# Kernel optimization log

Hardware: AMD Instinct MI355X
Metric: run time of the kernel (lower is better)

Reference implementation:

```python
import jax, jax.numpy as jnp
import numpy as np


def setup_inputs() -> dict:
    key = jax.random.key(0)
    k1, k2 = jax.random.split(key)
    B, N, M, D = 4, 8192, 8192, 3
    prediction = jax.random.normal(k1, (B, N, D), dtype=jnp.float32)
    target = jax.random.normal(k2, (B, M, D), dtype=jnp.float32)
    return {"prediction": prediction, "target": target}


def reference(prediction, target):
    # prediction: [B, N, 3], target: [B, M, 3] (already channels-last,
    # matching the module's transpose-if-needed behavior).
    x2 = jnp.sum(prediction * prediction, axis=-1)  # [B, N]
    y2 = jnp.sum(target * target, axis=-1)          # [B, M]
    xy = jnp.einsum('bnd,bmd->bnm', prediction, target)  # [B, N, M]
    d2 = x2[:, :, None] + y2[:, None, :] - 2.0 * xy
    d2 = jnp.maximum(d2, 0.0)  # numerical guard
    # pytorch3d chamfer_distance defaults: point_reduction='mean',
    # batch_reduction='mean' -> mean over points per direction, mean over batch,
    # then sum the two directions.
    cham_x = jnp.min(d2, axis=2).mean()  # pred -> target
    cham_y = jnp.min(d2, axis=1).mean()  # target -> pred
    return cham_x + cham_y
```

## Files before the change

### kernel.cpp

```cpp
#include <hip/hip_runtime.h>


#define BLOCK 256
#define RPT   8
#define MC    256
#define NPTS  8192
#define NCH   (NPTS / MC)
#define NB    4

typedef float v2f __attribute__((ext_vector_type(2)));
typedef float v4f __attribute__((ext_vector_type(4)));

__device__ __forceinline__ float min3f(float a, float b, float c) {
    float d;
    asm("v_min3_f32 %0, %1, %2, %3" : "=v"(d) : "v"(a), "v"(b), "v"(c));
    return d;
}

__device__ __forceinline__ v2f pk_fma(v2f a, v2f b, v2f c) {
    v2f d;
    asm("v_pk_fma_f32 %0, %1, %2, %3" : "=v"(d) : "v"(a), "v"(b), "v"(c));
    return d;
}

__global__ __launch_bounds__(BLOCK) void chamfer_min_fused(
    const float* __restrict__ pred, const float* __restrict__ targ,
    float* __restrict__ pA,
    float* __restrict__ pB,
    double* __restrict__ acc, unsigned int* __restrict__ counter) {
    if (blockIdx.x == 0 && blockIdx.y == 0 && blockIdx.z == 0 && threadIdx.x == 0) {
        *acc = 0.0;
        *counter = 0u;
    }

    const int z   = blockIdx.z;
    const int dir = z >> 2, b = z & (NB - 1);
    const float* X = dir ? targ : pred;
    const float* Y = dir ? pred : targ;
    float* partial = dir ? pB : pA;

    __shared__ v4f ldsA[MC / 2];
    __shared__ v4f ldsB[MC / 2];
    const int mc = blockIdx.y;

    if (threadIdx.x < MC / 2) {
        const int p = threadIdx.x;
        const float* yp = Y + ((size_t)b * NPTS + (size_t)mc * MC + 2 * p) * 3;
        float ax = yp[0], ay = yp[1], az = yp[2];
        float bx = yp[3], by = yp[4], bz = yp[5];
        float aw = fmaf(ax, ax, fmaf(ay, ay, az * az));
        float bw = fmaf(bx, bx, fmaf(by, by, bz * bz));
        ldsA[p] = (v4f){ax, bx, ay, by};
        ldsB[p] = (v4f){az, bz, aw, bw};
    }
    __syncthreads();

    const int row0 = blockIdx.x * (BLOCK * RPT);
    v2f qx[RPT], qy[RPT], qz[RPT];
    float x2[RPT], best[RPT];
#pragma unroll
    for (int r = 0; r < RPT; ++r) {
        int row = row0 + r * BLOCK + threadIdx.x;
        const float* xp = X + ((size_t)b * NPTS + row) * 3;
        float px = xp[0], py = xp[1], pz = xp[2];
        qx[r] = (v2f){-2.0f * px, -2.0f * px};
        qy[r] = (v2f){-2.0f * py, -2.0f * py};
        qz[r] = (v2f){-2.0f * pz, -2.0f * pz};
        x2[r] = fmaf(px, px, fmaf(py, py, pz * pz));
        best[r] = 3.0e38f;
    }

#pragma unroll 2
    for (int j = 0; j < MC / 2; j += 2) {
        v4f A0 = ldsA[j],     B0 = ldsB[j];
        v4f A1 = ldsA[j + 1], B1 = ldsB[j + 1];
        v2f x01 = __builtin_shufflevector(A0, A0, 0, 1);
        v2f y01 = __builtin_shufflevector(A0, A0, 2, 3);
        v2f z01 = __builtin_shufflevector(B0, B0, 0, 1);
        v2f w01 = __builtin_shufflevector(B0, B0, 2, 3);
        v2f x23 = __builtin_shufflevector(A1, A1, 0, 1);
        v2f y23 = __builtin_shufflevector(A1, A1, 2, 3);
        v2f z23 = __builtin_shufflevector(B1, B1, 0, 1);
        v2f w23 = __builtin_shufflevector(B1, B1, 2, 3);
#pragma unroll
        for (int r = 0; r < RPT; ++r) {
            v2f c01 = pk_fma(qx[r], x01, pk_fma(qy[r], y01, pk_fma(qz[r], z01, w01)));
            v2f c23 = pk_fma(qx[r], x23, pk_fma(qy[r], y23, pk_fma(qz[r], z23, w23)));
            best[r] = min3f(best[r], c01.x, c01.y);
            best[r] = min3f(best[r], c23.x, c23.y);
        }
    }

#pragma unroll
    for (int r = 0; r < RPT; ++r) {
        int row = row0 + r * BLOCK + threadIdx.x;
        partial[((size_t)b * NCH + mc) * NPTS + row] = fmaxf(best[r] + x2[r], 0.0f);
    }
}

__global__ __launch_bounds__(256) void chamfer_reduce(
    const float* __restrict__ pA, const float* __restrict__ pB,
    double* __restrict__ acc, unsigned int* __restrict__ counter,
    float* __restrict__ out) {
    const int g = blockIdx.x * 256 + threadIdx.x;
    const int r4 = g * 4;
    const int half = NB * NPTS;
    const float* src = (r4 < half) ? pA : pB;
    const int gg = r4 & (half - 1);
    const int b = gg >> 13, r = gg & (NPTS - 1);

    v4f vb = (v4f){3.0e38f, 3.0e38f, 3.0e38f, 3.0e38f};
#pragma unroll 8
    for (int c = 0; c < NCH; ++c) {
        v4f v = *(const v4f*)(src + ((size_t)b * NCH + c) * NPTS + r);
        vb.x = fminf(vb.x, v.x);
        vb.y = fminf(vb.y, v.y);
        vb.z = fminf(vb.z, v.z);
        vb.w = fminf(vb.w, v.w);
    }

    double d = (double)vb.x + (double)vb.y + (double)vb.z + (double)vb.w;
    for (int off = 32; off > 0; off >>= 1) d += __shfl_down(d, off);
    __shared__ double sh[4];
    const int lane = threadIdx.x & 63, wid = threadIdx.x >> 6;
    if (lane == 0) sh[wid] = d;
    __syncthreads();

    if (threadIdx.x == 0) {
        double blocktotal = sh[0] + sh[1] + sh[2] + sh[3];
        atomicAdd(acc, blocktotal);
        __threadfence();
        unsigned int ticket = atomicAdd(counter, 1u);
        if (ticket == gridDim.x - 1) {
            __threadfence();
            double s = atomicAdd(acc, 0.0);
            out[0] = (float)(s / (double)(NB * NPTS));
        }
    }
}

extern "C" void kernel_launch(void* const* d_in, const int* in_sizes, int n_in,
                              void* d_out, int out_size, void* d_ws, size_t ws_size,
                              hipStream_t stream) {
    const float* pred = (const float*)d_in[0];
    const float* targ = (const float*)d_in[1];
    float* out = (float*)d_out;

    float* pA = (float*)d_ws;
    float* pB = pA + (size_t)NB * NCH * NPTS;
    double* acc = (double*)(pB + (size_t)NB * NCH * NPTS);
    unsigned int* counter = (unsigned int*)(acc + 1);

    dim3 g1(NPTS / (BLOCK * RPT), NCH, 2 * NB);
    chamfer_min_fused<<<g1, BLOCK, 0, stream>>>(pred, targ, pA, pB, acc, counter);

    const int nblk = (2 * NB * NPTS / 4) / 256;
    chamfer_reduce<<<nblk, 256, 0, stream>>>(pA, pB, acc, counter, out);
}
```

Before: 99.83 us.

## Pre-pack target points and stream them via scalar loads instead of LDS

Adds a pack kernel that precomputes squared norms and interleaves each group of four points into 64-byte records in workspace. The main kernel then drops its LDS staging and barrier, and streams these records into SGPRs with double-buffered s_load_dwordx16 so the packed FMAs take scalar operands. The aim is to remove LDS read traffic and the block sync from the inner loop. The cost is an extra kernel launch and explicit waitcnt serialisation on scalar loads every group.

```diff
diff --git a/kernel.cpp b/kernel.cpp
--- a/kernel.cpp
+++ b/kernel.cpp
@@ -7,53 +7,66 @@
 #define NPTS  8192
 #define NCH   (NPTS / MC)
 #define NB    4
+#define NGRP  (NPTS / 4)
+#define GPC   (MC / 4)
 
-typedef float v2f __attribute__((ext_vector_type(2)));
-typedef float v4f __attribute__((ext_vector_type(4)));
+typedef float v2f  __attribute__((ext_vector_type(2)));
+typedef float v4f  __attribute__((ext_vector_type(4)));
+typedef int   v16i __attribute__((ext_vector_type(16)));
 
 __device__ __forceinline__ float min3f(float a, float b, float c) {
     float d;
     asm("v_min3_f32 %0, %1, %2, %3" : "=v"(d) : "v"(a), "v"(b), "v"(c));
     return d;
 }
-
-__device__ __forceinline__ v2f pk_fma(v2f a, v2f b, v2f c) {
+__device__ __forceinline__ v2f pk_fma_vvs(v2f a, v2f b, v2f c) {
     v2f d;
-    asm("v_pk_fma_f32 %0, %1, %2, %3" : "=v"(d) : "v"(a), "v"(b), "v"(c));
+    asm("v_pk_fma_f32 %0, %1, %2, %3" : "=v"(d) : "v"(a), "v"(b), "s"(c));
+    return d;
+}
+__device__ __forceinline__ v2f pk_fma_vsv(v2f a, v2f b, v2f c) {
+    v2f d;
+    asm("v_pk_fma_f32 %0, %1, %2, %3" : "=v"(d) : "v"(a), "s"(b), "v"(c));
     return d;
 }
 
-__global__ __launch_bounds__(BLOCK) void chamfer_min_fused(
+__global__ __launch_bounds__(256) void pack_kernel(
     const float* __restrict__ pred, const float* __restrict__ targ,
+    float* __restrict__ pk, double* __restrict__ acc,
+    unsigned int* __restrict__ counter) {
+    const int t = blockIdx.x * 256 + threadIdx.x;
+    if (t == 0) { *acc = 0.0; *counter = 0u; }
+    const int dir = t / (NB * NGRP);
+    const int rem = t % (NB * NGRP);
+    const int b = rem / NGRP, g = rem % NGRP;
+    const float* Y = dir ? pred : targ;
+    const float* yp = Y + ((size_t)b * NPTS + (size_t)g * 4) * 3;
+    float out[16];
+#pragma unroll
+    for (int i = 0; i < 4; ++i) {
+        float x = yp[3 * i], y = yp[3 * i + 1], z = yp[3 * i + 2];
+        float w = fmaf(x, x, fmaf(y, y, z * z));
+        int base = (i >> 1) * 8, sub = i & 1;
+        out[base + 0 + sub] = x;
+        out[base + 2 + sub] = y;
+        out[base + 4 + sub] = w;
+        out[base + 6 + sub] = z;
+    }
+    v4f* dst = (v4f*)(pk + (size_t)t * 16);
+    const v4f* o = (const v4f*)out;
+    dst[0] = o[0]; dst[1] = o[1]; dst[2] = o[2]; dst[3] = o[3];
+}
+
+__global__ __launch_bounds__(BLOCK) void chamfer_min_smem(
+    const float* __restrict__ pred, const float* __restrict__ targ,
+    const float* __restrict__ pk,
     float* __restrict__ pA,
-    float* __restrict__ pB,
-    double* __restrict__ acc, unsigned int* __restrict__ counter) {
-    if (blockIdx.x == 0 && blockIdx.y == 0 && blockIdx.z == 0 && threadIdx.x == 0) {
-        *acc = 0.0;
-        *counter = 0u;
-    }
-
-    const int z   = blockIdx.z;
+    float* __restrict__ pB) {
+    const int z = blockIdx.z;
     const int dir = z >> 2, b = z & (NB - 1);
     const float* X = dir ? targ : pred;
-    const float* Y = dir ? pred : targ;
     float* partial = dir ? pB : pA;
-
-    __shared__ v4f ldsA[MC / 2];
-    __shared__ v4f ldsB[MC / 2];
     const int mc = blockIdx.y;
-
-    if (threadIdx.x < MC / 2) {
-        const int p = threadIdx.x;
-        const float* yp = Y + ((size_t)b * NPTS + (size_t)mc * MC + 2 * p) * 3;
-        float ax = yp[0], ay = yp[1], az = yp[2];
-        float bx = yp[3], by = yp[4], bz = yp[5];
-        float aw = fmaf(ax, ax, fmaf(ay, ay, az * az));
-        float bw = fmaf(bx, bx, fmaf(by, by, bz * bz));
-        ldsA[p] = (v4f){ax, bx, ay, by};
-        ldsB[p] = (v4f){az, bz, aw, bw};
-    }
-    __syncthreads();
 
     const int row0 = blockIdx.x * (BLOCK * RPT);
     v2f qx[RPT], qy[RPT], qz[RPT];
@@ -70,26 +83,39 @@
         best[r] = 3.0e38f;
     }
 
-#pragma unroll 2
-    for (int j = 0; j < MC / 2; j += 2) {
-        v4f A0 = ldsA[j],     B0 = ldsB[j];
-        v4f A1 = ldsA[j + 1], B1 = ldsB[j + 1];
-        v2f x01 = __builtin_shufflevector(A0, A0, 0, 1);
-        v2f y01 = __builtin_shufflevector(A0, A0, 2, 3);
-        v2f z01 = __builtin_shufflevector(B0, B0, 0, 1);
-        v2f w01 = __builtin_shufflevector(B0, B0, 2, 3);
-        v2f x23 = __builtin_shufflevector(A1, A1, 0, 1);
-        v2f y23 = __builtin_shufflevector(A1, A1, 2, 3);
-        v2f z23 = __builtin_shufflevector(B1, B1, 0, 1);
-        v2f w23 = __builtin_shufflevector(B1, B1, 2, 3);
-#pragma unroll
-        for (int r = 0; r < RPT; ++r) {
-            v2f c01 = pk_fma(qx[r], x01, pk_fma(qy[r], y01, pk_fma(qz[r], z01, w01)));
-            v2f c23 = pk_fma(qx[r], x23, pk_fma(qy[r], y23, pk_fma(qz[r], z23, w23)));
-            best[r] = min3f(best[r], c01.x, c01.y);
-            best[r] = min3f(best[r], c23.x, c23.y);
-        }
+#define AS2(S, i, j) (v2f){__int_as_float(S[i]), __int_as_float(S[j])}
+#define COMPUTE(S) do {                                                   \
+        v2f x01 = AS2(S, 0, 1),  y01 = AS2(S, 2, 3);                      \
+        v2f w01 = AS2(S, 4, 5),  z01 = AS2(S, 6, 7);                      \
+        v2f x23 = AS2(S, 8, 9),  y23 = AS2(S, 10, 11);                    \
+        v2f w23 = AS2(S, 12, 13), z23 = AS2(S, 14, 15);                   \
+        _Pragma("unroll")                                                 \
+        for (int r = 0; r < RPT; ++r) {                                   \
+            v2f t0 = pk_fma_vvs(qz[r], z01, w01);                         \
+            t0 = pk_fma_vsv(qy[r], y01, t0);                              \
+            t0 = pk_fma_vsv(qx[r], x01, t0);                              \
+            v2f t1 = pk_fma_vvs(qz[r], z23, w23);                         \
+            t1 = pk_fma_vsv(qy[r], y23, t1);                              \
+            t1 = pk_fma_vsv(qx[r], x23, t1);                              \
+            best[r] = min3f(best[r], t0.x, t0.y);                         \
+            best[r] = min3f(best[r], t1.x, t1.y);                         \
+        }                                                                 \
+    } while (0)
+
+    const float* base = pk + (((size_t)dir * NB + b) * NGRP + (size_t)mc * GPC) * 16;
+    v16i cur, nxt;
+    asm volatile("s_load_dwordx16 %0, %1, 0x0" : "=s"(cur) : "s"(base));
+    asm volatile("s_waitcnt lgkmcnt(0)" ::: "memory");
+    __builtin_amdgcn_sched_barrier(0);
+    for (int j = 0; j < GPC - 1; ++j) {
+        asm volatile("s_load_dwordx16 %0, %1, 0x40" : "=s"(nxt) : "s"(base));
+        COMPUTE(cur);
+        asm volatile("s_waitcnt lgkmcnt(0)" ::: "memory");
+        __builtin_amdgcn_sched_barrier(0);
+        cur = nxt;
+        base += 16;
     }
+    COMPUTE(cur);
 
 #pragma unroll
     for (int r = 0; r < RPT; ++r) {
@@ -148,11 +174,14 @@
 
     float* pA = (float*)d_ws;
     float* pB = pA + (size_t)NB * NCH * NPTS;
-    double* acc = (double*)(pB + (size_t)NB * NCH * NPTS);
+    float* pk = pB + (size_t)NB * NCH * NPTS;
+    double* acc = (double*)(pk + (size_t)2 * NB * NGRP * 16);
     unsigned int* counter = (unsigned int*)(acc + 1);
 
+    pack_kernel<<<(2 * NB * NGRP) / 256, 256, 0, stream>>>(pred, targ, pk, acc, counter);
+
     dim3 g1(NPTS / (BLOCK * RPT), NCH, 2 * NB);
-    chamfer_min_fused<<<g1, BLOCK, 0, stream>>>(pred, targ, pA, pB, acc, counter);
+    chamfer_min_smem<<<g1, BLOCK, 0, stream>>>(pred, targ, pk, pA, pB);
 
     const int nblk = (2 * NB * NPTS / 4) / 256;
     chamfer_reduce<<<nblk, 256, 0, stream>>>(pA, pB, acc, counter, out);
```

Measured after the change: 108.8 us. 1.09x slower.

## Broadcast query coords via op_sel and double rows per thread

Applied to the files above, without the earlier changes.

Each query point is now packed into two v2f registers, and v_pk_fma_f32 op_sel/op_sel_hi broadcasts one component to both lanes. This drops the duplicated -2x/-2y/-2z pairs and the separate x2 array. The freed registers let each thread handle 16 rows instead of 8, while the target chunk shrinks from 256 to 128 points, so the block count stays the same. The goal is more FMA work per LDS load. The cost is twice as many chunk partials, which doubles the partial buffer the reduce kernel has to read.

```diff
diff --git a/kernel.cpp b/kernel.cpp
--- a/kernel.cpp
+++ b/kernel.cpp
@@ -2,8 +2,8 @@
 
 
 #define BLOCK 256
-#define RPT   8
-#define MC    256
+#define RPT   16
+#define MC    128
 #define NPTS  8192
 #define NCH   (NPTS / MC)
 #define NB    4
@@ -16,10 +16,16 @@
     asm("v_min3_f32 %0, %1, %2, %3" : "=v"(d) : "v"(a), "v"(b), "v"(c));
     return d;
 }
-
-__device__ __forceinline__ v2f pk_fma(v2f a, v2f b, v2f c) {
+__device__ __forceinline__ v2f pk_fma_bl(v2f P, v2f b, v2f c) {
     v2f d;
-    asm("v_pk_fma_f32 %0, %1, %2, %3" : "=v"(d) : "v"(a), "v"(b), "v"(c));
+    asm("v_pk_fma_f32 %0, %1, %2, %3 op_sel:[0,0,0] op_sel_hi:[0,1,1]"
+        : "=v"(d) : "v"(P), "v"(b), "v"(c));
+    return d;
+}
+__device__ __forceinline__ v2f pk_fma_bh(v2f P, v2f b, v2f c) {
+    v2f d;
+    asm("v_pk_fma_f32 %0, %1, %2, %3 op_sel:[1,0,0] op_sel_hi:[1,1,1]"
+        : "=v"(d) : "v"(P), "v"(b), "v"(c));
     return d;
 }
 
@@ -56,17 +62,16 @@
     __syncthreads();
 
     const int row0 = blockIdx.x * (BLOCK * RPT);
-    v2f qx[RPT], qy[RPT], qz[RPT];
-    float x2[RPT], best[RPT];
+    v2f Pxy[RPT];
+    v2f Pzw[RPT];
+    float best[RPT];
 #pragma unroll
     for (int r = 0; r < RPT; ++r) {
         int row = row0 + r * BLOCK + threadIdx.x;
         const float* xp = X + ((size_t)b * NPTS + row) * 3;
         float px = xp[0], py = xp[1], pz = xp[2];
-        qx[r] = (v2f){-2.0f * px, -2.0f * px};
-        qy[r] = (v2f){-2.0f * py, -2.0f * py};
-        qz[r] = (v2f){-2.0f * pz, -2.0f * pz};
-        x2[r] = fmaf(px, px, fmaf(py, py, pz * pz));
+        Pxy[r] = (v2f){-2.0f * px, -2.0f * py};
+        Pzw[r] = (v2f){-2.0f * pz, fmaf(px, px, fmaf(py, py, pz * pz))};
         best[r] = 3.0e38f;
     }
 
@@ -84,17 +89,21 @@
         v2f w23 = __builtin_shufflevector(B1, B1, 2, 3);
 #pragma unroll
         for (int r = 0; r < RPT; ++r) {
-            v2f c01 = pk_fma(qx[r], x01, pk_fma(qy[r], y01, pk_fma(qz[r], z01, w01)));
-            v2f c23 = pk_fma(qx[r], x23, pk_fma(qy[r], y23, pk_fma(qz[r], z23, w23)));
-            best[r] = min3f(best[r], c01.x, c01.y);
-            best[r] = min3f(best[r], c23.x, c23.y);
+            v2f t0 = pk_fma_bl(Pzw[r], z01, w01);
+            t0 = pk_fma_bh(Pxy[r], y01, t0);
+            t0 = pk_fma_bl(Pxy[r], x01, t0);
+            v2f t1 = pk_fma_bl(Pzw[r], z23, w23);
+            t1 = pk_fma_bh(Pxy[r], y23, t1);
+            t1 = pk_fma_bl(Pxy[r], x23, t1);
+            best[r] = min3f(best[r], t0.x, t0.y);
+            best[r] = min3f(best[r], t1.x, t1.y);
         }
     }
 
 #pragma unroll
     for (int r = 0; r < RPT; ++r) {
         int row = row0 + r * BLOCK + threadIdx.x;
-        partial[((size_t)b * NCH + mc) * NPTS + row] = fmaxf(best[r] + x2[r], 0.0f);
+        partial[((size_t)b * NCH + mc) * NPTS + row] = fmaxf(best[r] + Pzw[r].y, 0.0f);
     }
 }
 
```

Result: slower. 111.0 us (+11.2%).
